# Optimization experiments

Hardware: AMD Instinct MI355X
Metric: run time of the kernel (lower is better)

Reference implementation:

```python
import jax, jax.numpy as jnp
import numpy as np

D_MODEL, NUM_HEADS, ROPE_DIM = 256, 8, 16
B_GRAPHS, N_MAX = 16, 512


def _make_batch():
    # ragged graph sizes between 256 and 512 atoms; contiguous, sorted ids
    sizes = np.array([256 + (i * 256) // 15 for i in range(B_GRAPHS)], dtype=np.int64)
    return np.repeat(np.arange(B_GRAPHS), sizes)  # total N = 6137


def setup_inputs() -> dict:
    key = jax.random.key(0)
    ks = jax.random.split(key, 6)
    batch_np = _make_batch()
    N = int(batch_np.shape[0])
    x = jax.random.normal(ks[0], (N, D_MODEL), jnp.float32)
    pos = jax.random.normal(ks[1], (N, 3), jnp.float32) * 3.0
    W_qkv = jax.random.normal(ks[2], (D_MODEL, 3 * D_MODEL), jnp.float32) / np.sqrt(D_MODEL).astype(np.float32)
    W_out = jax.random.normal(ks[3], (D_MODEL, D_MODEL), jnp.float32) / np.sqrt(D_MODEL).astype(np.float32)
    rope_freqs = jax.random.normal(ks[4], (ROPE_DIM,), jnp.float32) * 0.1
    W_rope = jax.random.normal(ks[5], (ROPE_DIM, NUM_HEADS), jnp.float32) / np.sqrt(ROPE_DIM).astype(np.float32)
    gamma = jnp.ones((D_MODEL,), jnp.float32)
    beta = jnp.zeros((D_MODEL,), jnp.float32)
    return {"x": x, "pos": pos, "batch": jnp.asarray(batch_np, jnp.int32),
            "W_qkv": W_qkv, "W_out": W_out, "rope_freqs": rope_freqs,
            "W_rope": W_rope, "gamma": gamma, "beta": beta,
            "B": B_GRAPHS, "n_max": N_MAX}


def _forward(x, pos, W_qkv, W_out, rope_freqs, W_rope, gamma, beta, batch, B, n_max):
    N, d = x.shape
    H = W_rope.shape[1]
    hd = d // H
    scale = hd ** -0.5
    # pad ragged graphs to [B, n_max] via vectorized scatter (batch is sorted)
    sizes = jax.ops.segment_sum(jnp.ones((N,), jnp.int32), batch, num_segments=B)
    offsets = jnp.concatenate([jnp.zeros((1,), jnp.int32), jnp.cumsum(sizes)[:-1].astype(jnp.int32)])
    pidx = jnp.arange(N, dtype=jnp.int32) - offsets[batch]  # position within graph
    x_pad = jnp.zeros((B, n_max, d), x.dtype).at[batch, pidx].set(x)
    pos_pad = jnp.zeros((B, n_max, 3), pos.dtype).at[batch, pidx].set(pos)
    pad = jnp.ones((B, n_max), bool).at[batch, pidx].set(False)  # True = padding
    # multi-head self-attention on scalar channel
    qkv = x_pad @ W_qkv  # [B, n, 3d]
    q, k, v = jnp.split(qkv, 3, axis=-1)
    heads = lambda t: t.reshape(B, n_max, H, hd).transpose(0, 2, 1, 3)  # [B,H,n,hd]
    q, k, v = heads(q), heads(k), heads(v)
    logits = jnp.einsum('bhid,bhjd->bhij', q, k) * scale
    # Euclidean RoPE distance bias: rope_proj(cos(|omega| * ||r_i - r_j||))
    diff = pos_pad[:, :, None, :] - pos_pad[:, None, :, :]  # [B,n,n,3]
    sq = jnp.sum(diff * diff, axis=-1)
    dist = jnp.where(sq > 0, jnp.sqrt(jnp.where(sq > 0, sq, 1.0)), 0.0)  # safe norm
    fourier = jnp.cos(dist[..., None] * jnp.abs(rope_freqs))  # [B,n,n,r]
    bias = jnp.einsum('bijr,rh->bhij', fourier, W_rope)
    pair_pad = (pad[:, :, None] | pad[:, None, :])[:, None]  # [B,1,n,n]
    bias = jnp.where(pair_pad, 0.0, bias)
    logits = jnp.where(pad[:, None, None, :], -1e9, logits + bias)
    attn = jax.nn.softmax(logits, axis=-1)
    out = jnp.einsum('bhij,bhjd->bhid', attn, v)
    out = out.transpose(0, 2, 1, 3).reshape(B, n_max, d) @ W_out
    out_flat = out[batch, pidx]  # gather back to flat node list
    # residual + LayerNorm (eps = 1e-5)
    y = x + out_flat
    mu = jnp.mean(y, axis=-1, keepdims=True)
    var = jnp.mean((y - mu) ** 2, axis=-1, keepdims=True)
    return gamma * (y - mu) * jax.lax.rsqrt(var + 1e-5) + beta


def reference(x, pos, batch, W_qkv, W_out, rope_freqs, W_rope, gamma, beta, B, n_max):
    return _forward(x, pos, W_qkv, W_out, rope_freqs, W_rope, gamma, beta, batch, B, n_max)
```

## Files before the change

### kernel.cpp

```cpp
#include <hip/hip_runtime.h>
#include <hip/hip_bf16.h>

typedef __hip_bfloat16 bf16;
typedef short bf16x8 __attribute__((ext_vector_type(8)));
typedef float f32x4 __attribute__((ext_vector_type(4)));

#define NGRAPH 16
#define QSCALE 0.17677669529663687f
#define VT_LD 8192

struct __align__(16) bf8x { bf16 v[8]; };

__device__ __forceinline__ float b2f(bf16 v) { return __bfloat162float(v); }

__device__ __forceinline__ bf16x8 ldcvt8(const float* p) {
  float4 u = *(const float4*)p, v = *(const float4*)(p + 4);
  __align__(16) bf16 tmp[8];
  tmp[0] = __float2bfloat16(u.x); tmp[1] = __float2bfloat16(u.y);
  tmp[2] = __float2bfloat16(u.z); tmp[3] = __float2bfloat16(u.w);
  tmp[4] = __float2bfloat16(v.x); tmp[5] = __float2bfloat16(v.y);
  tmp[6] = __float2bfloat16(v.z); tmp[7] = __float2bfloat16(v.w);
  return *(const bf16x8*)tmp;
}

__global__ __launch_bounds__(256) void k_pre(const float* __restrict__ Wqkv,
                                             const float* __restrict__ Wout,
                                             const int* __restrict__ batch,
                                             bf16* __restrict__ Wqkv_t,
                                             bf16* __restrict__ Wout_t,
                                             int* __restrict__ offs, int N) {
  __shared__ float ld[64][65];
  int bid = blockIdx.x, t = threadIdx.x;
  int c = t & 63, r0 = t >> 6;
  if (bid < 48) {
    int k0 = (bid & 3) * 64, n0 = (bid >> 2) * 64;
    #pragma unroll
    for (int r = r0; r < 64; r += 4) ld[r][c] = Wqkv[(size_t)(k0 + r) * 768 + n0 + c];
    __syncthreads();
    #pragma unroll
    for (int r = r0; r < 64; r += 4)
      Wqkv_t[(size_t)(n0 + r) * 256 + k0 + c] = __float2bfloat16(ld[c][r]);
  } else if (bid < 64) {
    int b2 = bid - 48;
    int k0 = (b2 & 3) * 64, n0 = (b2 >> 2) * 64;
    #pragma unroll
    for (int r = r0; r < 64; r += 4) ld[r][c] = Wout[(size_t)(k0 + r) * 256 + n0 + c];
    __syncthreads();
    #pragma unroll
    for (int r = r0; r < 64; r += 4)
      Wout_t[(size_t)(n0 + r) * 256 + k0 + c] = __float2bfloat16(ld[c][r]);
  } else {
    for (int i = t; i < N; i += 256) {
      if (i == 0) { offs[0] = 0; offs[NGRAPH] = N; }
      else if (batch[i] != batch[i - 1]) offs[batch[i]] = i;
    }
  }
}

__global__ __launch_bounds__(256) void k_gemm(const float* __restrict__ x,
                                              const bf16* __restrict__ Wqkv_t,
                                              const int* __restrict__ batch,
                                              const int* __restrict__ offs,
                                              bf16* __restrict__ QKVb,
                                              bf16* __restrict__ VT, int N) {
  __shared__ float tr[64][65];
  __shared__ int rowcol[64];
  int t = threadIdx.x;
  int w = t >> 6, l = t & 63, fr = l & 15, fq = l >> 4;
  int m0 = blockIdx.x * 64, n0 = blockIdx.y * 64;
  if (t < 64) {
    int m = m0 + t; if (m > N - 1) m = N - 1;
    int b = batch[m];
    rowcol[t] = b * 512 + (m - offs[b]);
  }
  int arow = m0 + w * 16 + fr; if (arow > N - 1) arow = N - 1;
  bf16x8 af[8];
  #pragma unroll
  for (int kt = 0; kt < 8; ++kt)
    af[kt] = ldcvt8(x + (size_t)arow * 256 + kt * 32 + fq * 8);
  #pragma unroll
  for (int p = 0; p < 3; ++p) {
    f32x4 acc[4];
    #pragma unroll
    for (int nt = 0; nt < 4; ++nt) {
      acc[nt] = (f32x4){0.f, 0.f, 0.f, 0.f};
      int brow = p * 256 + n0 + nt * 16 + fr;
      #pragma unroll
      for (int kt = 0; kt < 8; ++kt) {
        bf16x8 bf_ = *(const bf16x8*)(Wqkv_t + (size_t)brow * 256 + kt * 32 + fq * 8);
        acc[nt] = __builtin_amdgcn_mfma_f32_16x16x32_bf16(af[kt], bf_, acc[nt], 0, 0, 0);
      }
    }
    float sc = (p == 0) ? QSCALE : 1.f;
    #pragma unroll
    for (int nt = 0; nt < 4; ++nt) {
      int col = p * 256 + n0 + nt * 16 + fr;
      #pragma unroll
      for (int rr = 0; rr < 4; ++rr) {
        int m = m0 + w * 16 + fq * 4 + rr;
        if (m < N) QKVb[(size_t)m * 768 + col] = __float2bfloat16(acc[nt][rr] * sc);
      }
    }
    if (p == 2) {
      #pragma unroll
      for (int nt = 0; nt < 4; ++nt)
        #pragma unroll
        for (int rr = 0; rr < 4; ++rr)
          tr[nt * 16 + fr][w * 16 + fq * 4 + rr] = acc[nt][rr];
      __syncthreads();
      int c = t >> 2, r0 = (t & 3) * 16;
      int dg = n0 + c;
      #pragma unroll
      for (int i = 0; i < 16; ++i) {
        int r = r0 + i;
        VT[(size_t)dg * VT_LD + rowcol[r]] = __float2bfloat16(tr[c][r]);
      }
    }
  }
}

__global__ __launch_bounds__(256) void k_attn(const float* __restrict__ pos,
                                              const float* __restrict__ freqs,
                                              const float* __restrict__ Wrope,
                                              const bf16* __restrict__ QKVb,
                                              const bf16* __restrict__ VT,
                                              const int* __restrict__ offs,
                                              float* __restrict__ Op,
                                              float* __restrict__ lp, int N) {
  __shared__ __align__(16) bf16 Tg[384][8];
  __shared__ __align__(16) bf16 Sbf[2][8][64][8];
  __shared__ __align__(16) bf16 Pt[4][16][40];
  int b = blockIdx.y, jc = blockIdx.z;
  int off = offs[b], n = offs[b + 1] - off;
  int q0 = blockIdx.x * 16;
  if (q0 >= n) return;
  int t = threadIdx.x, w = t >> 6, l = t & 63, fr = l & 15, fq = l >> 4;

  for (int i = t; i < 384; i += 256) {
    float d = i * 0.125f;
    float a[8];
    #pragma unroll
    for (int h = 0; h < 8; ++h) a[h] = 0.f;
    #pragma unroll
    for (int r = 0; r < 16; ++r) {
      float cv = __cosf(d * fabsf(freqs[r]));
      #pragma unroll
      for (int h = 0; h < 8; ++h) a[h] += cv * Wrope[r * 8 + h];
    }
    __align__(16) bf16 row[8];
    #pragma unroll
    for (int h = 0; h < 8; ++h) row[h] = __float2bfloat16(a[h]);
    *(bf16x8*)&Tg[i][0] = *(const bf16x8*)row;
  }

  int h0 = w, h1 = w + 4;
  const bf16* Kb0 = QKVb + (size_t)off * 768 + 256 + h0 * 32 + fq * 8;
  const bf16* Kb1 = QKVb + (size_t)off * 768 + 256 + h1 * 32 + fq * 8;
  const bf16* Vb0 = VT + (size_t)(h0 * 32 + fr) * VT_LD + b * 512 + fq * 8;
  const bf16* Vb1 = VT + (size_t)(h1 * 32 + fr) * VT_LD + b * 512 + fq * 8;
  int qrow = q0 + fr; bool qv = qrow < n;
  size_t qoff = (size_t)(qv ? off + qrow : off) * 768 + fq * 8;
  bf16x8 aq[2];
  aq[0] = *(const bf16x8*)(QKVb + qoff + h0 * 32);
  aq[1] = *(const bf16x8*)(QKVb + qoff + h1 * 32);
  if (!qv) { aq[0] = (bf16x8){0,0,0,0,0,0,0,0}; aq[1] = aq[0]; }

  int bq = t >> 5, bj = t & 31;
  float qpx[2], qpy[2], qpz[2]; bool bqv[2];
  #pragma unroll
  for (int e = 0; e < 2; ++e) {
    int qq = q0 + bq + 8 * e; bqv[e] = qq < n;
    int a = (bqv[e] ? off + qq : off) * 3;
    qpx[e] = pos[a]; qpy[e] = pos[a + 1]; qpz[e] = pos[a + 2];
  }

  f32x4 Oa[2][2];
  Oa[0][0] = (f32x4){0.f,0.f,0.f,0.f}; Oa[0][1] = Oa[0][0];
  Oa[1][0] = Oa[0][0];                 Oa[1][1] = Oa[0][0];
  float lacc[2][4] = {{0.f,0.f,0.f,0.f},{0.f,0.f,0.f,0.f}};
  int jtiles = (n + 31) >> 5;
  int jt0 = (jtiles * jc) >> 1, jt1 = (jtiles * (jc + 1)) >> 1;

  auto produce = [&](int JT, int BUF) {
    int jg = JT * 32 + bj; bool vj = jg < n;
    int a = (vj ? off + jg : off) * 3;
    float jx = pos[a], jy = pos[a + 1], jz = pos[a + 2];
    #pragma unroll
    for (int e = 0; e < 2; ++e) {
      int q = bq + 8 * e;
      int L = (q >> 2) * 16 + (bj & 15);
      int k = (bj >> 4) * 4 + (q & 3);
      if (vj && bqv[e]) {
        float dx = qpx[e] - jx, dy = qpy[e] - jy, dz = qpz[e] - jz;
        float d = sqrtf(dx * dx + dy * dy + dz * dz);
        float fi = d * 8.0f;
        int i = (int)fi; if (i > 382) i = 382;
        float fr2 = fi - (float)i;
        bf8x t0 = *(const bf8x*)&Tg[i][0];
        bf8x t1 = *(const bf8x*)&Tg[i + 1][0];
        #pragma unroll
        for (int h = 0; h < 8; ++h) {
          float u0 = b2f(t0.v[h]);
          float bv = u0 + fr2 * (b2f(t1.v[h]) - u0);
          Sbf[BUF][h][L][k] = __float2bfloat16(bv);
        }
      } else {
        bf16 s = __float2bfloat16(vj ? 0.f : -1e30f);
        #pragma unroll
        for (int h = 0; h < 8; ++h) Sbf[BUF][h][L][k] = s;
      }
    }
  };

  bf16x8 ck[2][2], cv[2][2];
  auto loadt = [&](int JT) {
    int k0 = JT * 32 + fr, k1 = k0 + 16;
    size_t r0 = (size_t)((k0 < n) ? k0 : 0) * 768;
    size_t r1 = (size_t)((k1 < n) ? k1 : 0) * 768;
    ck[0][0] = *(const bf16x8*)(Kb0 + r0); ck[0][1] = *(const bf16x8*)(Kb0 + r1);
    ck[1][0] = *(const bf16x8*)(Kb1 + r0); ck[1][1] = *(const bf16x8*)(Kb1 + r1);
    cv[0][0] = *(const bf16x8*)(Vb0 + JT * 32);
    cv[0][1] = *(const bf16x8*)(Vb0 + (size_t)16 * VT_LD + JT * 32);
    cv[1][0] = *(const bf16x8*)(Vb1 + JT * 32);
    cv[1][1] = *(const bf16x8*)(Vb1 + (size_t)16 * VT_LD + JT * 32);
  };

  __syncthreads();
  produce(jt0, 0);
  __syncthreads();
  for (int jt = jt0; jt < jt1; ++jt) {
    int par = (jt - jt0) & 1;
    loadt(jt);
    if (jt + 1 < jt1) produce(jt + 1, par ^ 1);
    #pragma unroll
    for (int hh = 0; hh < 2; ++hh) {
      int h = w + 4 * hh;
      f32x4 z = {0.f, 0.f, 0.f, 0.f};
      f32x4 S0 = __builtin_amdgcn_mfma_f32_16x16x32_bf16(aq[hh], ck[hh][0], z, 0, 0, 0);
      f32x4 S1 = __builtin_amdgcn_mfma_f32_16x16x32_bf16(aq[hh], ck[hh][1], z, 0, 0, 0);
      bf8x bb = *(const bf8x*)&Sbf[par][h][l][0];
      #pragma unroll
      for (int k = 0; k < 8; ++k) {
        int jti = k >> 2, rr = k & 3;
        float s = (jti ? S1[rr] : S0[rr]) + b2f(bb.v[k]);
        float p = __expf(s);
        lacc[hh][rr] += p;
        Pt[w][fq * 4 + rr][jti * 16 + fr] = __float2bfloat16(p);
      }
      bf16x8 ap = *(const bf16x8*)&Pt[w][fr][fq * 8];
      Oa[hh][0] = __builtin_amdgcn_mfma_f32_16x16x32_bf16(ap, cv[hh][0], Oa[hh][0], 0, 0, 0);
      Oa[hh][1] = __builtin_amdgcn_mfma_f32_16x16x32_bf16(ap, cv[hh][1], Oa[hh][1], 0, 0, 0);
    }
    __syncthreads();
  }
  #pragma unroll
  for (int hh = 0; hh < 2; ++hh)
    #pragma unroll
    for (int rr = 0; rr < 4; ++rr) {
      #pragma unroll
      for (int m2 = 1; m2 <= 8; m2 <<= 1) lacc[hh][rr] += __shfl_xor(lacc[hh][rr], m2);
    }
  float* Opc = Op + (size_t)jc * N * 256;
  float* lpc = lp + (size_t)jc * N * 8;
  #pragma unroll
  for (int hh = 0; hh < 2; ++hh) {
    int h = w + 4 * hh;
    #pragma unroll
    for (int rr = 0; rr < 4; ++rr) {
      int row = q0 + fq * 4 + rr;
      if (row < n) {
        #pragma unroll
        for (int dh = 0; dh < 2; ++dh)
          Opc[(size_t)(off + row) * 256 + h * 32 + dh * 16 + fr] = Oa[hh][dh][rr];
        if (fr == 0) lpc[(size_t)(off + row) * 8 + h] = lacc[hh][rr];
      }
    }
  }
}

__global__ __launch_bounds__(256) void k_out_ln(const float* __restrict__ Op,
                                                const float* __restrict__ lp,
                                                const bf16* __restrict__ Bt,
                                                const float* __restrict__ x,
                                                const float* __restrict__ gamma,
                                                const float* __restrict__ beta,
                                                float* __restrict__ out, int M) {
  __shared__ float ps[4][16], pss[4][16];
  int t = threadIdx.x, w = t >> 6, l = t & 63, fr = l & 15, fq = l >> 4;
  int m0 = blockIdx.x * 16;
  int arow = m0 + fr; if (arow > M - 1) arow = M - 1;
  const float* Op0 = Op;
  const float* Op1 = Op + (size_t)M * 256;
  float linv[8];
  {
    float4 a0 = *(const float4*)(lp + (size_t)arow * 8);
    float4 a1 = *(const float4*)(lp + (size_t)arow * 8 + 4);
    float4 b0 = *(const float4*)(lp + (size_t)(M + arow) * 8);
    float4 b1 = *(const float4*)(lp + (size_t)(M + arow) * 8 + 4);
    linv[0] = 1.f / (a0.x + b0.x); linv[1] = 1.f / (a0.y + b0.y);
    linv[2] = 1.f / (a0.z + b0.z); linv[3] = 1.f / (a0.w + b0.w);
    linv[4] = 1.f / (a1.x + b1.x); linv[5] = 1.f / (a1.y + b1.y);
    linv[6] = 1.f / (a1.z + b1.z); linv[7] = 1.f / (a1.w + b1.w);
  }
  bf16x8 af[8];
  #pragma unroll
  for (int kt = 0; kt < 8; ++kt) {
    size_t o = (size_t)arow * 256 + kt * 32 + fq * 8;
    float4 u0 = *(const float4*)(Op0 + o), v0 = *(const float4*)(Op0 + o + 4);
    float4 u1 = *(const float4*)(Op1 + o), v1 = *(const float4*)(Op1 + o + 4);
    float li = linv[kt];
    __align__(16) bf16 tmp[8];
    tmp[0] = __float2bfloat16((u0.x + u1.x) * li);
    tmp[1] = __float2bfloat16((u0.y + u1.y) * li);
    tmp[2] = __float2bfloat16((u0.z + u1.z) * li);
    tmp[3] = __float2bfloat16((u0.w + u1.w) * li);
    tmp[4] = __float2bfloat16((v0.x + v1.x) * li);
    tmp[5] = __float2bfloat16((v0.y + v1.y) * li);
    tmp[6] = __float2bfloat16((v0.z + v1.z) * li);
    tmp[7] = __float2bfloat16((v0.w + v1.w) * li);
    af[kt] = *(const bf16x8*)tmp;
  }
  f32x4 acc[4];
  #pragma unroll
  for (int nt = 0; nt < 4; ++nt) {
    acc[nt] = (f32x4){0.f, 0.f, 0.f, 0.f};
    int brow = w * 64 + nt * 16 + fr;
    #pragma unroll
    for (int kt = 0; kt < 8; ++kt) {
      bf16x8 bf_ = *(const bf16x8*)(Bt + (size_t)brow * 256 + kt * 32 + fq * 8);
      acc[nt] = __builtin_amdgcn_mfma_f32_16x16x32_bf16(af[kt], bf_, acc[nt], 0, 0, 0);
    }
  }
  float y[4][4];
  #pragma unroll
  for (int rr = 0; rr < 4; ++rr) {
    int row = m0 + fq * 4 + rr;
    int rc = (row < M) ? row : (M - 1);
    float s = 0.f, ss = 0.f;
    #pragma unroll
    for (int nt = 0; nt < 4; ++nt) {
      float v = acc[nt][rr] + x[(size_t)rc * 256 + w * 64 + nt * 16 + fr];
      y[rr][nt] = v; s += v; ss += v * v;
    }
    #pragma unroll
    for (int m2 = 1; m2 <= 8; m2 <<= 1) { s += __shfl_xor(s, m2); ss += __shfl_xor(ss, m2); }
    if (fr == 0) { ps[w][fq * 4 + rr] = s; pss[w][fq * 4 + rr] = ss; }
  }
  __syncthreads();
  #pragma unroll
  for (int rr = 0; rr < 4; ++rr) {
    int row = m0 + fq * 4 + rr;
    int ri = fq * 4 + rr;
    float s = ps[0][ri] + ps[1][ri] + ps[2][ri] + ps[3][ri];
    float ss = pss[0][ri] + pss[1][ri] + pss[2][ri] + pss[3][ri];
    float mean = s * (1.f / 256.f);
    float var = ss * (1.f / 256.f) - mean * mean;
    float rstd = rsqrtf(var + 1e-5f);
    if (row < M) {
      #pragma unroll
      for (int nt = 0; nt < 4; ++nt) {
        int col = w * 64 + nt * 16 + fr;
        out[(size_t)row * 256 + col] = gamma[col] * (y[rr][nt] - mean) * rstd + beta[col];
      }
    }
  }
}

extern "C" void kernel_launch(void* const* d_in, const int* in_sizes, int n_in,
                              void* d_out, int out_size, void* d_ws, size_t ws_size,
                              hipStream_t stream) {
  (void)n_in; (void)out_size; (void)ws_size;
  const float* x     = (const float*)d_in[0];
  const float* pos   = (const float*)d_in[1];
  const int*   batch = (const int*)d_in[2];
  const float* Wqkv  = (const float*)d_in[3];
  const float* Wout  = (const float*)d_in[4];
  const float* freqs = (const float*)d_in[5];
  const float* Wrope = (const float*)d_in[6];
  const float* gamma = (const float*)d_in[7];
  const float* beta  = (const float*)d_in[8];
  float* out = (float*)d_out;

  int N = in_sizes[0] / 256;

  char* base = (char*)d_ws;
  int*   offs   = (int*)base;
  bf16*  QKVb   = (bf16*)(base + 1024);
  bf16*  VT     = (bf16*)(base + 9427456);
  bf16*  Wqkv_t = (bf16*)(base + 13621760);
  bf16*  Wout_t = (bf16*)(base + 14014976);
  float* Op     = (float*)(base + 14146048);
  float* lp     = (float*)(base + 26714624);

  int MBm = (N + 63) / 64;
  k_pre<<<65, 256, 0, stream>>>(Wqkv, Wout, batch, Wqkv_t, Wout_t, offs, N);
  k_gemm<<<dim3(MBm, 4), 256, 0, stream>>>(x, Wqkv_t, batch, offs, QKVb, VT, N);
  k_attn<<<dim3(32, NGRAPH, 2), 256, 0, stream>>>(pos, freqs, Wrope, QKVb, VT, offs, Op, lp, N);
  k_out_ln<<<(N + 15) / 16, 256, 0, stream>>>(Op, lp, Wout_t, x, gamma, beta, out, N);
}
```

Baseline: 178.5 us.

## Precompute RoPE bias table once, compute bias per-lane, split keys four ways

Moves the distance-to-bias lookup table build out of every attention block into a single pre-kernel block, storing adjacent table entries packed per head. Each lane now computes its own bias values in registers for the MFMA accumulator layout instead of a shared-memory producer/consumer double buffer, which removes the per-tile __syncthreads. The key dimension is split across four blocks instead of two, raising parallelism. In exchange the partial-output buffer and the reduction in the output kernel double, and the redundant distance and sqrt computations per lane increase.

```diff
diff --git a/kernel.cpp b/kernel.cpp
--- a/kernel.cpp
+++ b/kernel.cpp
@@ -9,9 +9,11 @@
 #define QSCALE 0.17677669529663687f
 #define VT_LD 8192
 
-struct __align__(16) bf8x { bf16 v[8]; };
-
 __device__ __forceinline__ float b2f(bf16 v) { return __bfloat162float(v); }
+__device__ __forceinline__ unsigned short f2bfu(float x) {
+  bf16 b = __float2bfloat16(x);
+  return *(unsigned short*)&b;
+}
 
 __device__ __forceinline__ bf16x8 ldcvt8(const float* p) {
   float4 u = *(const float4*)p, v = *(const float4*)(p + 4);
@@ -25,10 +27,13 @@
 
 __global__ __launch_bounds__(256) void k_pre(const float* __restrict__ Wqkv,
                                              const float* __restrict__ Wout,
+                                             const float* __restrict__ freqs,
+                                             const float* __restrict__ Wrope,
                                              const int* __restrict__ batch,
                                              bf16* __restrict__ Wqkv_t,
                                              bf16* __restrict__ Wout_t,
-                                             int* __restrict__ offs, int N) {
+                                             int* __restrict__ offs,
+                                             unsigned* __restrict__ tbl, int N) {
   __shared__ float ld[64][65];
   int bid = blockIdx.x, t = threadIdx.x;
   int c = t & 63, r0 = t >> 6;
@@ -49,10 +54,35 @@
     #pragma unroll
     for (int r = r0; r < 64; r += 4)
       Wout_t[(size_t)(n0 + r) * 256 + k0 + c] = __float2bfloat16(ld[c][r]);
-  } else {
+  } else if (bid == 64) {
     for (int i = t; i < N; i += 256) {
       if (i == 0) { offs[0] = 0; offs[NGRAPH] = N; }
       else if (batch[i] != batch[i - 1]) offs[batch[i]] = i;
+    }
+  } else {
+    __shared__ float Bv[8][388];
+    for (int i = t; i < 385; i += 256) {
+      float d = i * 0.125f;
+      float a[8];
+      #pragma unroll
+      for (int h = 0; h < 8; ++h) a[h] = 0.f;
+      #pragma unroll
+      for (int r = 0; r < 16; ++r) {
+        float cv = __cosf(d * fabsf(freqs[r]));
+        #pragma unroll
+        for (int h = 0; h < 8; ++h) a[h] += cv * Wrope[r * 8 + h];
+      }
+      #pragma unroll
+      for (int h = 0; h < 8; ++h) Bv[h][i] = a[h];
+    }
+    __syncthreads();
+    for (int idx = t; idx < 8 * 384; idx += 256) {
+      int h = idx >> 8 | 0;
+      h = idx / 384;
+      int i = idx - h * 384;
+      unsigned lo = f2bfu(Bv[h][i]);
+      unsigned hi = f2bfu(Bv[h][i + 1]);
+      tbl[idx] = lo | (hi << 16);
     }
   }
 }
@@ -120,40 +150,24 @@
 }
 
 __global__ __launch_bounds__(256) void k_attn(const float* __restrict__ pos,
-                                              const float* __restrict__ freqs,
-                                              const float* __restrict__ Wrope,
+                                              const unsigned* __restrict__ tbl,
                                               const bf16* __restrict__ QKVb,
                                               const bf16* __restrict__ VT,
                                               const int* __restrict__ offs,
                                               float* __restrict__ Op,
                                               float* __restrict__ lp, int N) {
-  __shared__ __align__(16) bf16 Tg[384][8];
-  __shared__ __align__(16) bf16 Sbf[2][8][64][8];
-  __shared__ __align__(16) bf16 Pt[4][16][40];
+  __shared__ unsigned Tp[8][384];
+  __shared__ __align__(16) bf16 Pt[4][2][16][40];
   int b = blockIdx.y, jc = blockIdx.z;
   int off = offs[b], n = offs[b + 1] - off;
   int q0 = blockIdx.x * 16;
   if (q0 >= n) return;
   int t = threadIdx.x, w = t >> 6, l = t & 63, fr = l & 15, fq = l >> 4;
-
-  for (int i = t; i < 384; i += 256) {
-    float d = i * 0.125f;
-    float a[8];
-    #pragma unroll
-    for (int h = 0; h < 8; ++h) a[h] = 0.f;
-    #pragma unroll
-    for (int r = 0; r < 16; ++r) {
-      float cv = __cosf(d * fabsf(freqs[r]));
-      #pragma unroll
-      for (int h = 0; h < 8; ++h) a[h] += cv * Wrope[r * 8 + h];
-    }
-    __align__(16) bf16 row[8];
-    #pragma unroll
-    for (int h = 0; h < 8; ++h) row[h] = __float2bfloat16(a[h]);
-    *(bf16x8*)&Tg[i][0] = *(const bf16x8*)row;
-  }
-
   int h0 = w, h1 = w + 4;
+
+  for (int i = t; i < 768; i += 256)
+    ((uint4*)Tp)[i] = ((const uint4*)tbl)[i];
+
   const bf16* Kb0 = QKVb + (size_t)off * 768 + 256 + h0 * 32 + fq * 8;
   const bf16* Kb1 = QKVb + (size_t)off * 768 + 256 + h1 * 32 + fq * 8;
   const bf16* Vb0 = VT + (size_t)(h0 * 32 + fr) * VT_LD + b * 512 + fq * 8;
@@ -165,13 +179,12 @@
   aq[1] = *(const bf16x8*)(QKVb + qoff + h1 * 32);
   if (!qv) { aq[0] = (bf16x8){0,0,0,0,0,0,0,0}; aq[1] = aq[0]; }
 
-  int bq = t >> 5, bj = t & 31;
-  float qpx[2], qpy[2], qpz[2]; bool bqv[2];
-  #pragma unroll
-  for (int e = 0; e < 2; ++e) {
-    int qq = q0 + bq + 8 * e; bqv[e] = qq < n;
-    int a = (bqv[e] ? off + qq : off) * 3;
-    qpx[e] = pos[a]; qpy[e] = pos[a + 1]; qpz[e] = pos[a + 2];
+  float qx[4], qy[4], qz[4]; bool qvv[4];
+  #pragma unroll
+  for (int rr = 0; rr < 4; ++rr) {
+    int qr = q0 + fq * 4 + rr; qvv[rr] = qr < n;
+    int a = (qvv[rr] ? off + qr : off) * 3;
+    qx[rr] = pos[a]; qy[rr] = pos[a + 1]; qz[rr] = pos[a + 2];
   }
 
   f32x4 Oa[2][2];
@@ -179,79 +192,79 @@
   Oa[1][0] = Oa[0][0];                 Oa[1][1] = Oa[0][0];
   float lacc[2][4] = {{0.f,0.f,0.f,0.f},{0.f,0.f,0.f,0.f}};
   int jtiles = (n + 31) >> 5;
-  int jt0 = (jtiles * jc) >> 1, jt1 = (jtiles * (jc + 1)) >> 1;
-
-  auto produce = [&](int JT, int BUF) {
-    int jg = JT * 32 + bj; bool vj = jg < n;
-    int a = (vj ? off + jg : off) * 3;
-    float jx = pos[a], jy = pos[a + 1], jz = pos[a + 2];
-    #pragma unroll
-    for (int e = 0; e < 2; ++e) {
-      int q = bq + 8 * e;
-      int L = (q >> 2) * 16 + (bj & 15);
-      int k = (bj >> 4) * 4 + (q & 3);
-      if (vj && bqv[e]) {
-        float dx = qpx[e] - jx, dy = qpy[e] - jy, dz = qpz[e] - jz;
-        float d = sqrtf(dx * dx + dy * dy + dz * dz);
-        float fi = d * 8.0f;
-        int i = (int)fi; if (i > 382) i = 382;
-        float fr2 = fi - (float)i;
-        bf8x t0 = *(const bf8x*)&Tg[i][0];
-        bf8x t1 = *(const bf8x*)&Tg[i + 1][0];
-        #pragma unroll
-        for (int h = 0; h < 8; ++h) {
-          float u0 = b2f(t0.v[h]);
-          float bv = u0 + fr2 * (b2f(t1.v[h]) - u0);
-          Sbf[BUF][h][L][k] = __float2bfloat16(bv);
-        }
-      } else {
-        bf16 s = __float2bfloat16(vj ? 0.f : -1e30f);
-        #pragma unroll
-        for (int h = 0; h < 8; ++h) Sbf[BUF][h][L][k] = s;
-      }
-    }
-  };
-
-  bf16x8 ck[2][2], cv[2][2];
-  auto loadt = [&](int JT) {
-    int k0 = JT * 32 + fr, k1 = k0 + 16;
+  int jt0 = (jtiles * jc) >> 2, jt1 = (jtiles * (jc + 1)) >> 2;
+
+  __syncthreads();
+  for (int jt = jt0; jt < jt1; ++jt) {
+    int k0 = jt * 32 + fr, k1 = k0 + 16;
     size_t r0 = (size_t)((k0 < n) ? k0 : 0) * 768;
     size_t r1 = (size_t)((k1 < n) ? k1 : 0) * 768;
-    ck[0][0] = *(const bf16x8*)(Kb0 + r0); ck[0][1] = *(const bf16x8*)(Kb0 + r1);
-    ck[1][0] = *(const bf16x8*)(Kb1 + r0); ck[1][1] = *(const bf16x8*)(Kb1 + r1);
-    cv[0][0] = *(const bf16x8*)(Vb0 + JT * 32);
-    cv[0][1] = *(const bf16x8*)(Vb0 + (size_t)16 * VT_LD + JT * 32);
-    cv[1][0] = *(const bf16x8*)(Vb1 + JT * 32);
-    cv[1][1] = *(const bf16x8*)(Vb1 + (size_t)16 * VT_LD + JT * 32);
-  };
-
-  __syncthreads();
-  produce(jt0, 0);
-  __syncthreads();
-  for (int jt = jt0; jt < jt1; ++jt) {
-    int par = (jt - jt0) & 1;
-    loadt(jt);
-    if (jt + 1 < jt1) produce(jt + 1, par ^ 1);
-    #pragma unroll
-    for (int hh = 0; hh < 2; ++hh) {
-      int h = w + 4 * hh;
+    bf16x8 ck00 = *(const bf16x8*)(Kb0 + r0), ck01 = *(const bf16x8*)(Kb0 + r1);
+    bf16x8 ck10 = *(const bf16x8*)(Kb1 + r0), ck11 = *(const bf16x8*)(Kb1 + r1);
+    bf16x8 cv00 = *(const bf16x8*)(Vb0 + jt * 32);
+    bf16x8 cv01 = *(const bf16x8*)(Vb0 + (size_t)16 * VT_LD + jt * 32);
+    bf16x8 cv10 = *(const bf16x8*)(Vb1 + jt * 32);
+    bf16x8 cv11 = *(const bf16x8*)(Vb1 + (size_t)16 * VT_LD + jt * 32);
+    float jx[2], jy[2], jz[2]; bool vj[2];
+    #pragma unroll
+    for (int jti = 0; jti < 2; ++jti) {
+      int jrow = jt * 32 + jti * 16 + fr;
+      vj[jti] = jrow < n;
+      int a = (vj[jti] ? off + jrow : off) * 3;
+      jx[jti] = pos[a]; jy[jti] = pos[a + 1]; jz[jti] = pos[a + 2];
+    }
+    float bias[2][8];
+    #pragma unroll
+    for (int jti = 0; jti < 2; ++jti)
+      #pragma unroll
+      for (int rr = 0; rr < 4; ++rr) {
+        int k = jti * 4 + rr;
+        if (vj[jti] && qvv[rr]) {
+          float dx = qx[rr] - jx[jti], dy = qy[rr] - jy[jti], dz = qz[rr] - jz[jti];
+          float d = sqrtf(dx * dx + dy * dy + dz * dz);
+          float fi = d * 8.0f;
+          int i = (int)fi; if (i > 383) i = 383;
+          float fr2 = fi - (float)i;
+          unsigned p0 = Tp[h0][i], p1 = Tp[h1][i];
+          float lo0 = __uint_as_float(p0 << 16), hi0 = __uint_as_float(p0 & 0xffff0000u);
+          float lo1 = __uint_as_float(p1 << 16), hi1 = __uint_as_float(p1 & 0xffff0000u);
+          bias[0][k] = lo0 + fr2 * (hi0 - lo0);
+          bias[1][k] = lo1 + fr2 * (hi1 - lo1);
+        } else {
+          float v = vj[jti] ? 0.f : -1e30f;
+          bias[0][k] = v; bias[1][k] = v;
+        }
+      }
+    {
       f32x4 z = {0.f, 0.f, 0.f, 0.f};
-      f32x4 S0 = __builtin_amdgcn_mfma_f32_16x16x32_bf16(aq[hh], ck[hh][0], z, 0, 0, 0);
-      f32x4 S1 = __builtin_amdgcn_mfma_f32_16x16x32_bf16(aq[hh], ck[hh][1], z, 0, 0, 0);
-      bf8x bb = *(const bf8x*)&Sbf[par][h][l][0];
+      f32x4 S0 = __builtin_amdgcn_mfma_f32_16x16x32_bf16(aq[0], ck00, z, 0, 0, 0);
+      f32x4 S1 = __builtin_amdgcn_mfma_f32_16x16x32_bf16(aq[0], ck01, z, 0, 0, 0);
       #pragma unroll
       for (int k = 0; k < 8; ++k) {
         int jti = k >> 2, rr = k & 3;
-        float s = (jti ? S1[rr] : S0[rr]) + b2f(bb.v[k]);
-        float p = __expf(s);
-        lacc[hh][rr] += p;
-        Pt[w][fq * 4 + rr][jti * 16 + fr] = __float2bfloat16(p);
-      }
-      bf16x8 ap = *(const bf16x8*)&Pt[w][fr][fq * 8];
-      Oa[hh][0] = __builtin_amdgcn_mfma_f32_16x16x32_bf16(ap, cv[hh][0], Oa[hh][0], 0, 0, 0);
-      Oa[hh][1] = __builtin_amdgcn_mfma_f32_16x16x32_bf16(ap, cv[hh][1], Oa[hh][1], 0, 0, 0);
-    }
-    __syncthreads();
+        float p = __expf((jti ? S1[rr] : S0[rr]) + bias[jti][0 * 0 + 0] * 0.f + bias[0][k]);
+        lacc[0][rr] += p;
+        Pt[w][0][fq * 4 + rr][jti * 16 + fr] = __float2bfloat16(p);
+      }
+      bf16x8 ap = *(const bf16x8*)&Pt[w][0][fr][fq * 8];
+      Oa[0][0] = __builtin_amdgcn_mfma_f32_16x16x32_bf16(ap, cv00, Oa[0][0], 0, 0, 0);
+      Oa[0][1] = __builtin_amdgcn_mfma_f32_16x16x32_bf16(ap, cv01, Oa[0][1], 0, 0, 0);
+    }
+    {
+      f32x4 z = {0.f, 0.f, 0.f, 0.f};
+      f32x4 S0 = __builtin_amdgcn_mfma_f32_16x16x32_bf16(aq[1], ck10, z, 0, 0, 0);
+      f32x4 S1 = __builtin_amdgcn_mfma_f32_16x16x32_bf16(aq[1], ck11, z, 0, 0, 0);
+      #pragma unroll
+      for (int k = 0; k < 8; ++k) {
+        int jti = k >> 2, rr = k & 3;
+        float p = __expf((jti ? S1[rr] : S0[rr]) + bias[1][k]);
+        lacc[1][rr] += p;
+        Pt[w][1][fq * 4 + rr][jti * 16 + fr] = __float2bfloat16(p);
+      }
+      bf16x8 ap = *(const bf16x8*)&Pt[w][1][fr][fq * 8];
+      Oa[1][0] = __builtin_amdgcn_mfma_f32_16x16x32_bf16(ap, cv10, Oa[1][0], 0, 0, 0);
+      Oa[1][1] = __builtin_amdgcn_mfma_f32_16x16x32_bf16(ap, cv11, Oa[1][1], 0, 0, 0);
+    }
   }
   #pragma unroll
   for (int hh = 0; hh < 2; ++hh)
@@ -289,35 +302,35 @@
   int t = threadIdx.x, w = t >> 6, l = t & 63, fr = l & 15, fq = l >> 4;
   int m0 = blockIdx.x * 16;
   int arow = m0 + fr; if (arow > M - 1) arow = M - 1;
-  const float* Op0 = Op;
-  const float* Op1 = Op + (size_t)M * 256;
+  float lsum[8];
+  #pragma unroll
+  for (int h = 0; h < 8; ++h) lsum[h] = 0.f;
+  #pragma unroll
+  for (int c = 0; c < 4; ++c) {
+    float4 a0 = *(const float4*)(lp + ((size_t)c * M + arow) * 8);
+    float4 a1 = *(const float4*)(lp + ((size_t)c * M + arow) * 8 + 4);
+    lsum[0] += a0.x; lsum[1] += a0.y; lsum[2] += a0.z; lsum[3] += a0.w;
+    lsum[4] += a1.x; lsum[5] += a1.y; lsum[6] += a1.z; lsum[7] += a1.w;
+  }
   float linv[8];
-  {
-    float4 a0 = *(const float4*)(lp + (size_t)arow * 8);
-    float4 a1 = *(const float4*)(lp + (size_t)arow * 8 + 4);
-    float4 b0 = *(const float4*)(lp + (size_t)(M + arow) * 8);
-    float4 b1 = *(const float4*)(lp + (size_t)(M + arow) * 8 + 4);
-    linv[0] = 1.f / (a0.x + b0.x); linv[1] = 1.f / (a0.y + b0.y);
-    linv[2] = 1.f / (a0.z + b0.z); linv[3] = 1.f / (a0.w + b0.w);
-    linv[4] = 1.f / (a1.x + b1.x); linv[5] = 1.f / (a1.y + b1.y);
-    linv[6] = 1.f / (a1.z + b1.z); linv[7] = 1.f / (a1.w + b1.w);
-  }
+  #pragma unroll
+  for (int h = 0; h < 8; ++h) linv[h] = 1.f / lsum[h];
   bf16x8 af[8];
   #pragma unroll
   for (int kt = 0; kt < 8; ++kt) {
     size_t o = (size_t)arow * 256 + kt * 32 + fq * 8;
-    float4 u0 = *(const float4*)(Op0 + o), v0 = *(const float4*)(Op0 + o + 4);
-    float4 u1 = *(const float4*)(Op1 + o), v1 = *(const float4*)(Op1 + o + 4);
+    float s[8] = {0.f,0.f,0.f,0.f,0.f,0.f,0.f,0.f};
+    #pragma unroll
+    for (int c = 0; c < 4; ++c) {
+      const float* Opc = Op + (size_t)c * M * 256;
+      float4 u = *(const float4*)(Opc + o), v = *(const float4*)(Opc + o + 4);
+      s[0] += u.x; s[1] += u.y; s[2] += u.z; s[3] += u.w;
+      s[4] += v.x; s[5] += v.y; s[6] += v.z; s[7] += v.w;
+    }
     float li = linv[kt];
     __align__(16) bf16 tmp[8];
-    tmp[0] = __float2bfloat16((u0.x + u1.x) * li);
-    tmp[1] = __float2bfloat16((u0.y + u1.y) * li);
-    tmp[2] = __float2bfloat16((u0.z + u1.z) * li);
-    tmp[3] = __float2bfloat16((u0.w + u1.w) * li);
-    tmp[4] = __float2bfloat16((v0.x + v1.x) * li);
-    tmp[5] = __float2bfloat16((v0.y + v1.y) * li);
-    tmp[6] = __float2bfloat16((v0.z + v1.z) * li);
-    tmp[7] = __float2bfloat16((v0.w + v1.w) * li);
+    #pragma unroll
+    for (int e = 0; e < 8; ++e) tmp[e] = __float2bfloat16(s[e] * li);
     af[kt] = *(const bf16x8*)tmp;
   }
   f32x4 acc[4];
@@ -384,17 +397,18 @@
   int N = in_sizes[0] / 256;
 
   char* base = (char*)d_ws;
-  int*   offs   = (int*)base;
-  bf16*  QKVb   = (bf16*)(base + 1024);
-  bf16*  VT     = (bf16*)(base + 9427456);
-  bf16*  Wqkv_t = (bf16*)(base + 13621760);
-  bf16*  Wout_t = (bf16*)(base + 14014976);
-  float* Op     = (float*)(base + 14146048);
-  float* lp     = (float*)(base + 26714624);
+  int*      offs   = (int*)base;
+  bf16*     QKVb   = (bf16*)(base + 1024);
+  bf16*     VT     = (bf16*)(base + 9427456);
+  bf16*     Wqkv_t = (bf16*)(base + 13621760);
+  bf16*     Wout_t = (bf16*)(base + 14014976);
+  unsigned* tbl    = (unsigned*)(base + 14146048);
+  float*    Op     = (float*)(base + 14158336);
+  float*    lp     = (float*)(base + 39295488);
 
   int MBm = (N + 63) / 64;
-  k_pre<<<65, 256, 0, stream>>>(Wqkv, Wout, batch, Wqkv_t, Wout_t, offs, N);
+  k_pre<<<66, 256, 0, stream>>>(Wqkv, Wout, freqs, Wrope, batch, Wqkv_t, Wout_t, offs, tbl, N);
   k_gemm<<<dim3(MBm, 4), 256, 0, stream>>>(x, Wqkv_t, batch, offs, QKVb, VT, N);
-  k_attn<<<dim3(32, NGRAPH, 2), 256, 0, stream>>>(pos, freqs, Wrope, QKVb, VT, offs, Op, lp, N);
+  k_attn<<<dim3(32, NGRAPH, 4), 256, 0, stream>>>(pos, tbl, QKVb, VT, offs, Op, lp, N);
   k_out_ln<<<(N + 15) / 16, 256, 0, stream>>>(Op, lp, Wout_t, x, gamma, beta, out, N);
 }
```

Measured after the change: 190.4 us. 6.7% more time.
